# Performance work log

Hardware: AMD Instinct MI355X
Metric: run time of the kernel (lower is better)

## Reference

```python
import jax, jax.numpy as jnp
import numpy as np

K = 20  # neighbors, from init kwarg k

def _knn_idx(x, k):
    # x: [B, C, N]; returns indices of k nearest neighbors [B, N, k]
    xx = jnp.sum(x * x, axis=1)                      # [B, N]
    inner = jnp.einsum('bcn,bcm->bnm', x, x)         # [B, N, N]
    neg_dist = 2.0 * inner - xx[:, :, None] - xx[:, None, :]
    return jax.lax.top_k(neg_dist, k)[1]


def _graph_feature(x, k):
    # x: [B, C, N] -> [B, N, k, 2C] = concat(neighbor - center, center)
    idx = _knn_idx(jax.lax.stop_gradient(x), k)
    xt = jnp.swapaxes(x, 1, 2)                       # [B, N, C]
    nb = jax.vmap(lambda pts, i: pts[i])(xt, idx)    # [B, N, k, C]
    ctr = jnp.broadcast_to(xt[:, :, None, :], nb.shape)
    return jnp.concatenate([nb - ctr, ctr], axis=-1)


def _edge_conv(x, layers, k):
    # x: [B, C, N]; layers: list of (w [Co,Ci], scale [Co], bias [Co])
    g = _graph_feature(x, k)                         # [B, N, k, 2C]
    for w, s, b in layers:
        g = jax.nn.leaky_relu(jnp.einsum('bnkc,oc->bnko', g, w) * s + b, 0.2)
    return jnp.swapaxes(jnp.max(g, axis=2), 1, 2)    # [B, Co, N]


def setup_inputs() -> dict:
    key = jax.random.key(0)
    ks = jax.random.split(key, 20)
    B, N = 2, 8192
    emb = 1024
    def w(k_, shape):
        fan_in = shape[1]
        return jax.random.normal(k_, shape, jnp.float32) * (1.0 / np.sqrt(fan_in))
    def sc(k_, c):
        return jax.random.uniform(k_, (c,), jnp.float32, 0.5, 1.5)
    def bi(k_, c):
        return jax.random.normal(k_, (c,), jnp.float32) * 0.1
    inp = {
        'points': jax.random.normal(ks[0], (B, N, 3), jnp.float32),
        'w1a': w(ks[1], (64, 12)),  's1a': sc(ks[2], 64),  'b1a': bi(ks[3], 64),
        'w1b': w(ks[4], (64, 64)),  's1b': sc(ks[5], 64),  'b1b': bi(ks[6], 64),
        'w2a': w(ks[7], (64, 128)), 's2a': sc(ks[8], 64),  'b2a': bi(ks[9], 64),
        'w2b': w(ks[10], (64, 64)), 's2b': sc(ks[11], 64), 'b2b': bi(ks[12], 64),
        'w3a': w(ks[13], (64, 128)),'s3a': sc(ks[14], 64), 'b3a': bi(ks[15], 64),
        'wg':  w(ks[16], (emb, 192)),'sg': sc(ks[17], emb),'bg': bi(ks[18], emb),
    }
    return inp


def reference(points, w1a, s1a, b1a, w1b, s1b, b1b,
              w2a, s2a, b2a, w2b, s2b, b2b,
              w3a, s3a, b3a, wg, sg, bg):
    B, N, _ = points.shape
    xyz = jnp.swapaxes(points, 1, 2)                 # [B, 3, N]
    x = jnp.concatenate([xyz, xyz], axis=1)          # [B, 6, N] (features == xyz when C==3)
    x1 = _edge_conv(x,  [(w1a, s1a, b1a), (w1b, s1b, b1b)], K)
    x2 = _edge_conv(x1, [(w2a, s2a, b2a), (w2b, s2b, b2b)], K)
    x3 = _edge_conv(x2, [(w3a, s3a, b3a)], K)
    cat = jnp.concatenate([x1, x2, x3], axis=1)      # [B, 192, N]
    h = jax.nn.leaky_relu(
        jnp.einsum('bcn,oc->bon', cat, wg) * sg[None, :, None] + bg[None, :, None], 0.2)
    g = jnp.max(h, axis=-1, keepdims=True)           # [B, emb, 1]
    x_max = jnp.broadcast_to(g, (B, h.shape[1], N))  # [B, emb, N]
    return x_max
```

## Files before the change

### kernel.cpp

```cpp
#include <hip/hip_runtime.h>
#include <hip/hip_bf16.h>

#define NPTS 8192
#define KNN  20
#define KC   4

__device__ __forceinline__ unsigned fkey(float f) {
  unsigned u = __float_as_uint(f);
  return (u & 0x80000000u) ? ~u : (u | 0x80000000u);
}
__device__ __forceinline__ float funkey(unsigned k) {
  return (k & 0x80000000u) ? __uint_as_float(k & 0x7fffffffu) : __uint_as_float(~k);
}
__device__ __forceinline__ float lrelu(float x) { return x >= 0.f ? x : 0.2f * x; }

__global__ __launch_bounds__(256) void prep_kernel(
    const float* __restrict__ w1a, const float* __restrict__ w1b,
    const float* __restrict__ w2a, const float* __restrict__ w2b,
    const float* __restrict__ w3a, const float* __restrict__ wg,
    float* __restrict__ wp1A, float* __restrict__ wp1B,
    float* __restrict__ wp2A, float* __restrict__ wp2B,
    float* __restrict__ wp3A, float* __restrict__ wgT)
{
  const int t0 = blockIdx.x * blockDim.x + threadIdx.x;
  const int NT = gridDim.x * blockDim.x;
  for (int f = t0; f < 512; f += NT) {
    int i = f & 3, o = (f >> 2) & 63, c4 = f >> 8, c = c4 * 4 + i;
    float v = 0.f;
    if (c < 3)      v = w1a[o*12 + c]     + w1a[o*12 + c + 3];
    else if (c < 6) v = w1a[o*12 + c + 3] + w1a[o*12 + c + 6];
    wp1A[f] = v;
  }
  for (int f = t0; f < 4096; f += NT) {
    int i = f & 3, o = (f >> 2) & 63, c4 = f >> 8, c = c4 * 4 + i;
    wp1B[f] = w1b[o*64 + c];
    wp2B[f] = w2b[o*64 + c];
  }
  for (int f = t0; f < 8192; f += NT) {
    int i = f & 3, o = (f >> 2) & 63, c4 = f >> 8, c = c4 * 4 + i;
    wp2A[f] = w2a[o*128 + c];
    wp3A[f] = w3a[o*128 + c];
  }
  for (int f = t0; f < 192 * 1024; f += NT) {
    int c = f >> 10, o = f & 1023;
    wgT[f] = wg[o*192 + c];
  }
}

__global__ __launch_bounds__(256) void xx_points(const float* __restrict__ pts,
                                                 float* __restrict__ xx)
{
  int t = blockIdx.x * 256 + threadIdx.x;
  if (t < 2 * NPTS) {
    const float* p = pts + (size_t)t * 3;
    xx[t] = p[0]*p[0] + p[1]*p[1] + p[2]*p[2];
  }
}

__device__ __forceinline__ void bitonic64_desc_f(float& v, int lane) {
  #pragma unroll
  for (int k = 2; k <= 64; k <<= 1) {
    #pragma unroll
    for (int j = k >> 1; j >= 1; j >>= 1) {
      float o = __shfl_xor(v, j);
      bool take_max = (((lane & k) == 0) == ((lane & j) == 0));
      v = take_max ? fmaxf(v, o) : fminf(v, o);
    }
  }
}

__device__ __forceinline__ void bitonic64_desc_u64(unsigned long long& v, int lane) {
  #pragma unroll
  for (int k = 2; k <= 64; k <<= 1) {
    #pragma unroll
    for (int j = k >> 1; j >= 1; j >>= 1) {
      unsigned long long o = __shfl_xor(v, j);
      bool take_max = (((lane & k) == 0) == ((lane & j) == 0));
      unsigned long long hi = v > o ? v : o;
      unsigned long long lo = v > o ? o : v;
      v = take_max ? hi : lo;
    }
  }
}

__device__ void sel20_half(float* __restrict__ sdh, int half, int lane,
                           float* __restrict__ hv, int* __restrict__ hj,
                           float* __restrict__ cv, int* __restrict__ cj)
{
  float m = -INFINITY;
  const float4* rp = (const float4*)(sdh + lane * 64);
  #pragma unroll
  for (int t = 0; t < 16; ++t) {
    float4 x = rp[(t + lane) & 15];
    m = fmaxf(m, fmaxf(fmaxf(x.x, x.y), fmaxf(x.z, x.w)));
  }
  bitonic64_desc_f(m, lane);
  float That = __shfl(m, 19);

  int base = 0;
  for (int i = 0; i < 64; ++i) {
    float v = sdh[i * 64 + lane];
    bool p = (v >= That);
    unsigned long long mk = __ballot(p);
    if (p) {
      int pos = base + (int)__popcll(mk & ((1ull << lane) - 1ull));
      if (pos < 64) { cv[pos] = v; cj[pos] = i * 64 + lane; }
    }
    base += (int)__popcll(mk);
  }

  if (base <= 64) {
    unsigned long long key = 0ull;
    if (lane < base)
      key = (((unsigned long long)fkey(cv[lane])) << 32) | (unsigned)(~cj[lane]);
    bitonic64_desc_u64(key, lane);
    if (lane < KNN) {
      hv[lane] = funkey((unsigned)(key >> 32));
      hj[lane] = (half << 12) + (int)((~(unsigned)key) & 4095u);
    }
  } else {
    for (int kk = 0; kk < KNN; ++kk) {
      float bv = -INFINITY; int bj = 4096;
      for (int i = 0; i < 64; ++i) {
        float v = sdh[i * 64 + lane];
        if (v > bv) { bv = v; bj = i * 64 + lane; }
      }
      #pragma unroll
      for (int mm = 32; mm >= 1; mm >>= 1) {
        float ov = __shfl_xor(bv, mm); int oj = __shfl_xor(bj, mm);
        if (ov > bv || (ov == bv && oj < bj)) { bv = ov; bj = oj; }
      }
      if (lane == 0) { hv[kk] = bv; hj[kk] = (half << 12) + bj; }
      sdh[bj] = -INFINITY;
    }
  }
}

__device__ __forceinline__ void merge_halves(const float* __restrict__ hv,
                                             const int* __restrict__ hj,
                                             int lane, int* __restrict__ orow)
{
  unsigned long long key = 0ull;
  if (lane < 2 * KNN)
    key = (((unsigned long long)fkey(hv[lane])) << 32) | (unsigned)(~hj[lane]);
  bitonic64_desc_u64(key, lane);
  if (lane < KNN) orow[lane] = (int)((~(unsigned)key) & (NPTS - 1));
}

__device__ unsigned long long sel20_quarter(float* __restrict__ sdq, int jbase,
                                            int lane, float* __restrict__ cv,
                                            int* __restrict__ cj)
{
  float m = -INFINITY;
  #pragma unroll 8
  for (int i = 0; i < 32; ++i) m = fmaxf(m, sdq[i * 64 + lane]);
  bitonic64_desc_f(m, lane);
  float That = __shfl(m, 19);

  int base = 0;
  for (int i = 0; i < 32; ++i) {
    float v = sdq[i * 64 + lane];
    bool p = (v >= That);
    unsigned long long mk = __ballot(p);
    if (p) {
      int pos = base + (int)__popcll(mk & ((1ull << lane) - 1ull));
      if (pos < 64) { cv[pos] = v; cj[pos] = jbase + i * 64 + lane; }
    }
    base += (int)__popcll(mk);
  }

  unsigned long long key = 0ull;
  if (base <= 64) {
    if (lane < base)
      key = (((unsigned long long)fkey(cv[lane])) << 32) | (unsigned)(~cj[lane]);
    bitonic64_desc_u64(key, lane);
  } else {
    for (int kk = 0; kk < KNN; ++kk) {
      float bv = -INFINITY; int bj = 2048;
      for (int i = 0; i < 32; ++i) {
        float v = sdq[i * 64 + lane];
        if (v > bv) { bv = v; bj = i * 64 + lane; }
      }
      #pragma unroll
      for (int mm = 32; mm >= 1; mm >>= 1) {
        float ov = __shfl_xor(bv, mm); int oj = __shfl_xor(bj, mm);
        if (ov > bv || (ov == bv && oj < bj)) { bv = ov; bj = oj; }
      }
      if (lane == kk)
        key = (((unsigned long long)fkey(bv)) << 32) | (unsigned)(~(jbase + bj));
      sdq[bj] = -INFINITY;
    }
  }
  return key;
}

__global__ __launch_bounds__(512, 4) void knn3_kernel(
    const float* __restrict__ pts, const float* __restrict__ xx,
    int* __restrict__ idxout)
{
  __shared__ __align__(16) float sd[4][4096];
  __shared__ float s_ctr[4][4];
  __shared__ float s_hv[4][2 * KNN];
  __shared__ int   s_hj[4][2 * KNN];
  __shared__ float s_cv[4][64];
  __shared__ int   s_cj[4][64];
  const int tid = threadIdx.x;
  const int b   = blockIdx.x / (NPTS / 4);
  const int r0  = (blockIdx.x % (NPTS / 4)) * 4;
  const size_t rowbase = (size_t)b * NPTS;

  for (int i = tid; i < 12; i += 512)
    s_ctr[i / 3][i % 3] = pts[(rowbase + r0 + i / 3) * 3 + i % 3];
  __syncthreads();

  const float xr0 = xx[rowbase + r0 + 0], xr1 = xx[rowbase + r0 + 1];
  const float xr2 = xx[rowbase + r0 + 2], xr3 = xx[rowbase + r0 + 3];
  const float c00 = s_ctr[0][0], c01 = s_ctr[0][1], c02 = s_ctr[0][2];
  const float c10 = s_ctr[1][0], c11 = s_ctr[1][1], c12 = s_ctr[1][2];
  const float c20 = s_ctr[2][0], c21 = s_ctr[2][1], c22 = s_ctr[2][2];
  const float c30 = s_ctr[3][0], c31 = s_ctr[3][1], c32 = s_ctr[3][2];
  const int wid = tid >> 6, lane = tid & 63;

  #pragma unroll 1
  for (int h = 0; h < 2; ++h) {
    for (int jl = tid; jl < 4096; jl += 512) {
      const int jg = (h << 12) + jl;
      const float* fj = pts + (rowbase + jg) * 3;
      const float f0 = fj[0], f1 = fj[1], f2 = fj[2];
      const float xj = xx[rowbase + jg];
      sd[0][jl] = 2.f*(f0*c00 + f1*c01 + f2*c02) - xr0 - xj;
      sd[1][jl] = 2.f*(f0*c10 + f1*c11 + f2*c12) - xr1 - xj;
      sd[2][jl] = 2.f*(f0*c20 + f1*c21 + f2*c22) - xr2 - xj;
      sd[3][jl] = 2.f*(f0*c30 + f1*c31 + f2*c32) - xr3 - xj;
    }
    __syncthreads();
    if (wid < 4)
      sel20_half(sd[wid], h, lane, &s_hv[wid][h * KNN], &s_hj[wid][h * KNN],
                 s_cv[wid], s_cj[wid]);
    __syncthreads();
  }
  if (wid < 4)
    merge_halves(s_hv[wid], s_hj[wid], lane, idxout + (rowbase + r0 + wid) * KNN);
}

#define ACC4(A, C) \
  A.x += v0.x*C.x + v1.x*C.y + v2.x*C.z + v3.x*C.w; \
  A.y += v0.y*C.x + v1.y*C.y + v2.y*C.z + v3.y*C.w; \
  A.z += v0.z*C.x + v1.z*C.y + v2.z*C.z + v3.z*C.w; \
  A.w += v0.w*C.x + v1.w*C.y + v2.w*C.z + v3.w*C.w;

__global__ __launch_bounds__(512, 4) void knn64_kernel(
    const float* __restrict__ featT, const float* __restrict__ xx,
    int* __restrict__ idxout)
{
  __shared__ __align__(16) float sd[8][2048];
  __shared__ __align__(16) float s_ctr[8][64];
  __shared__ float s_cv[8][64];
  __shared__ int   s_cj[8][64];
  const int tid = threadIdx.x;
  const int bid = blockIdx.x;
  const int b   = (bid & 7) >> 2;
  const int r0  = (((bid >> 3) << 2) + (bid & 3)) * 8;
  const size_t tb = (size_t)b * 64 * NPTS;
  const size_t rowbase = (size_t)b * NPTS;

  s_ctr[tid >> 6][tid & 63] = featT[tb + (size_t)(tid & 63) * NPTS + r0 + (tid >> 6)];
  __syncthreads();

  const int wid = tid >> 6, lane = tid & 63;
  float xr[8];
  #pragma unroll
  for (int r = 0; r < 8; ++r) xr[r] = xx[rowbase + r0 + r];
  const float4* ct0 = (const float4*)s_ctr[0];
  const float4* ct1 = (const float4*)s_ctr[1];
  const float4* ct2 = (const float4*)s_ctr[2];
  const float4* ct3 = (const float4*)s_ctr[3];
  const float4* ct4 = (const float4*)s_ctr[4];
  const float4* ct5 = (const float4*)s_ctr[5];
  const float4* ct6 = (const float4*)s_ctr[6];
  const float4* ct7 = (const float4*)s_ctr[7];

  unsigned long long runkey = 0ull;

  #pragma unroll 1
  for (int h = 0; h < 4; ++h) {
    const int jl = (wid << 8) + (lane << 2);
    const int jg = (h << 11) + jl;
    float4 a0 = {0.f,0.f,0.f,0.f}, a1 = a0, a2 = a0, a3 = a0;
    float4 a4 = a0, a5 = a0, a6 = a0, a7 = a0;
    const float* fp0 = featT + tb + jg;
    #pragma unroll 2
    for (int c4 = 0; c4 < 16; ++c4) {
      const float* fp = fp0 + (size_t)(c4 * 4) * NPTS;
      float4 v0 = *(const float4*)(fp);
      float4 v1 = *(const float4*)(fp + NPTS);
      float4 v2 = *(const float4*)(fp + 2 * NPTS);
      float4 v3 = *(const float4*)(fp + 3 * NPTS);
      float4 c;
      c = ct0[c4]; ACC4(a0, c);
      c = ct1[c4]; ACC4(a1, c);
      c = ct2[c4]; ACC4(a2, c);
      c = ct3[c4]; ACC4(a3, c);
      c = ct4[c4]; ACC4(a4, c);
      c = ct5[c4]; ACC4(a5, c);
      c = ct6[c4]; ACC4(a6, c);
      c = ct7[c4]; ACC4(a7, c);
    }
    const float4 xv = *(const float4*)(xx + rowbase + jg);
    float4 s;
    #define STORE_ROW(A, R) \
      s.x = 2.f*A.x - xr[R] - xv.x; s.y = 2.f*A.y - xr[R] - xv.y; \
      s.z = 2.f*A.z - xr[R] - xv.z; s.w = 2.f*A.w - xr[R] - xv.w; \
      *(float4*)&sd[R][jl] = s;
    STORE_ROW(a0, 0); STORE_ROW(a1, 1); STORE_ROW(a2, 2); STORE_ROW(a3, 3);
    STORE_ROW(a4, 4); STORE_ROW(a5, 5); STORE_ROW(a6, 6); STORE_ROW(a7, 7);
    #undef STORE_ROW
    __syncthreads();

    unsigned long long pk = sel20_quarter(sd[wid], h << 11, lane,
                                          s_cv[wid], s_cj[wid]);
    unsigned long long nk = __shfl(pk, lane - 20);
    unsigned long long mkey = (lane < 20) ? runkey
                            : ((lane < 40) ? nk : 0ull);
    bitonic64_desc_u64(mkey, lane);
    runkey = mkey;
    __syncthreads();
  }
  if (lane < KNN)
    idxout[(rowbase + r0 + wid) * KNN + lane] =
        (int)((~(unsigned)runkey) & (NPTS - 1));
}

template<int D, bool HASB, bool WAUX>
__global__ __launch_bounds__(512, 2) void fused_conv(
    const float* __restrict__ feat, int fstride, int foff,
    const int* __restrict__ idx,
    const float4* __restrict__ wAp, const float* __restrict__ sa, const float* __restrict__ ba,
    const float4* __restrict__ wBp, const float* __restrict__ sb, const float* __restrict__ bb,
    float* __restrict__ outbuf, int ooff, float* __restrict__ xxout,
    float* __restrict__ featT)
{
  constexpr int CHA  = (D == 64) ? 32 : 2;
  constexpr int CHA4 = CHA * 4;
  __shared__ float4 s_wA[CHA * 64];
  __shared__ float4 s_wB[HASB ? 16 * 64 : 1];
  __shared__ __align__(16) float4 s_g[8 * KC * CHA];
  __shared__ __align__(16) float  s_h1[HASB ? 8 * KC * 64 : 4];
  __shared__ float s_ctr[8][(D > 4) ? D : 4];
  __shared__ float s_sa[64], s_ba[64], s_sb[64], s_bb[64];

  const int tid = threadIdx.x;
  const int p = tid >> 6, o = tid & 63;
  const int b  = blockIdx.x / (NPTS / 8);
  const int p0 = (blockIdx.x % (NPTS / 8)) * 8;
  const size_t rowbase = (size_t)b * NPTS;

  for (int i = tid; i < CHA * 64; i += 512) s_wA[i] = wAp[i];
  if (HASB) for (int i = tid; i < 16 * 64; i += 512) s_wB[i] = wBp[i];
  if (tid < 64) {
    s_sa[tid] = sa[tid]; s_ba[tid] = ba[tid];
    if (HASB) { s_sb[tid] = sb[tid]; s_bb[tid] = bb[tid]; }
  }
  for (int i = tid; i < 8 * D; i += 512)
    s_ctr[i / D][i % D] = feat[(rowbase + p0 + (i / D)) * fstride + foff + (i % D)];
  __syncthreads();

  float* s_gf = (float*)s_g;
  float hmax = -INFINITY;
  for (int kc = 0; kc < KNN / KC; ++kc) {
    for (int s = tid; s < 8 * KC * CHA4; s += 512) {
      int pp = s / (KC * CHA4);
      int rr = s - pp * (KC * CHA4);
      int kk = rr / CHA4;
      int c  = rr - kk * CHA4;
      int nb = idx[(rowbase + p0 + pp) * KNN + kc * KC + kk];
      float v;
      if (D == 64) {
        v = (c < 64) ? (feat[(rowbase + nb) * fstride + foff + c] - s_ctr[pp][c])
                     : s_ctr[pp][c - 64];
      } else {
        if (c < 3)      v = feat[(rowbase + nb) * 3 + c] - s_ctr[pp][c];
        else if (c < 6) v = s_ctr[pp][c - 3];
        else            v = 0.f;
      }
      s_gf[s] = v;
    }
    __syncthreads();

    float acc[KC];
    #pragma unroll
    for (int kk = 0; kk < KC; ++kk) acc[kk] = 0.f;
    for (int c4 = 0; c4 < CHA; ++c4) {
      float4 w = s_wA[c4 * 64 + o];
      #pragma unroll
      for (int kk = 0; kk < KC; ++kk) {
        float4 g = s_g[(p * KC + kk) * CHA + c4];
        acc[kk] += w.x*g.x + w.y*g.y + w.z*g.z + w.w*g.w;
      }
    }
    if (HASB) {
      #pragma unroll
      for (int kk = 0; kk < KC; ++kk)
        s_h1[(p * KC + kk) * 64 + o] = lrelu(acc[kk] * s_sa[o] + s_ba[o]);
      __syncthreads();
      float acc2[KC];
      #pragma unroll
      for (int kk = 0; kk < KC; ++kk) acc2[kk] = 0.f;
      const float4* s_h14 = (const float4*)s_h1;
      for (int c4 = 0; c4 < 16; ++c4) {
        float4 w = s_wB[c4 * 64 + o];
        #pragma unroll
        for (int kk = 0; kk < KC; ++kk) {
          float4 h = s_h14[(p * KC + kk) * 16 + c4];
          acc2[kk] += w.x*h.x + w.y*h.y + w.z*h.z + w.w*h.w;
        }
      }
      #pragma unroll
      for (int kk = 0; kk < KC; ++kk)
        hmax = fmaxf(hmax, lrelu(acc2[kk] * s_sb[o] + s_bb[o]));
      __syncthreads();
    } else {
      #pragma unroll
      for (int kk = 0; kk < KC; ++kk)
        hmax = fmaxf(hmax, lrelu(acc[kk] * s_sa[o] + s_ba[o]));
      __syncthreads();
    }
  }
  outbuf[(rowbase + p0 + p) * 192 + ooff + o] = hmax;
  if (WAUX) {
    featT[(size_t)b * 64 * NPTS + (size_t)o * NPTS + (p0 + p)] = hmax;
    float ss = hmax * hmax;
    #pragma unroll
    for (int m = 1; m < 64; m <<= 1) ss += __shfl_xor(ss, m);
    if (o == 0) xxout[rowbase + p0 + p] = ss;
  }
}

__global__ __launch_bounds__(256) void init_gmax(unsigned* __restrict__ g)
{
  int t = blockIdx.x * 256 + threadIdx.x;
  if (t < 2048) g[t] = fkey(-1e30f);
}

__global__ __launch_bounds__(256) void final_kernel(
    const float* __restrict__ cat, const float* __restrict__ wgT,
    const float* __restrict__ sg, const float* __restrict__ bg,
    unsigned* __restrict__ gmax)
{
  const int tid = threadIdx.x;
  const int chunk = blockIdx.x & 15;
  const int grp   = blockIdx.x >> 4;
  const int pt = grp * 256 + tid;
  const int b  = pt >> 13;
  const float4* crow = (const float4*)(cat + (size_t)pt * 192);
  float acc[64];
  #pragma unroll
  for (int o = 0; o < 64; ++o) acc[o] = 0.f;
  for (int c4 = 0; c4 < 48; ++c4) {
    float4 cv = crow[c4];
    const float* w0 = wgT + (size_t)(c4 * 4) * 1024 + chunk * 64;
    const float* w1 = w0 + 1024;
    const float* w2 = w1 + 1024;
    const float* w3 = w2 + 1024;
    #pragma unroll
    for (int o = 0; o < 64; ++o)
      acc[o] += cv.x*w0[o] + cv.y*w1[o] + cv.z*w2[o] + cv.w*w3[o];
  }
  const int lane = tid & 63;
  #pragma unroll
  for (int o = 0; o < 64; ++o) {
    int ch = chunk * 64 + o;
    float h = lrelu(acc[o] * sg[ch] + bg[ch]);
    #pragma unroll
    for (int m = 1; m < 64; m <<= 1) h = fmaxf(h, __shfl_xor(h, m));
    if (lane == 0) atomicMax(&gmax[b * 1024 + ch], fkey(h));
  }
}

__global__ __launch_bounds__(256) void bcast_kernel(const unsigned* __restrict__ gmax,
                                                    float* __restrict__ out)
{
  int t = blockIdx.x * 256 + threadIdx.x;
  int bo = t >> 11;
  float v = funkey(gmax[bo]);
  float4 w; w.x = v; w.y = v; w.z = v; w.w = v;
  ((float4*)out)[t] = w;
}

extern "C" void kernel_launch(void* const* d_in, const int* in_sizes, int n_in,
                              void* d_out, int out_size, void* d_ws, size_t ws_size,
                              hipStream_t stream)
{
  const float* points = (const float*)d_in[0];
  const float* w1a = (const float*)d_in[1];  const float* s1a = (const float*)d_in[2];  const float* b1a = (const float*)d_in[3];
  const float* w1b = (const float*)d_in[4];  const float* s1b = (const float*)d_in[5];  const float* b1b = (const float*)d_in[6];
  const float* w2a = (const float*)d_in[7];  const float* s2a = (const float*)d_in[8];  const float* b2a = (const float*)d_in[9];
  const float* w2b = (const float*)d_in[10]; const float* s2b = (const float*)d_in[11]; const float* b2b = (const float*)d_in[12];
  const float* w3a = (const float*)d_in[13]; const float* s3a = (const float*)d_in[14]; const float* b3a = (const float*)d_in[15];
  const float* wg  = (const float*)d_in[16]; const float* sg  = (const float*)d_in[17]; const float* bg  = (const float*)d_in[18];

  char* ws = (char*)d_ws;
  float*    cat   = (float*)(ws);
  float*    xxbuf = (float*)(ws + 12582912);
  int*      idxb  = (int*)  (ws + 12648448);
  float*    wp1A  = (float*)(ws + 13959168);
  float*    wp1B  = (float*)(ws + 13961216);
  float*    wp2A  = (float*)(ws + 13977600);
  float*    wp2B  = (float*)(ws + 14010368);
  float*    wp3A  = (float*)(ws + 14026752);
  float*    wgT   = (float*)(ws + 14059520);
  unsigned* gmax  = (unsigned*)(ws + 14845952);
  const size_t WS_NEED = 14854144;
  if (ws_size < WS_NEED || n_in != 19) return;

  float* featT = (float*)d_out;

  prep_kernel<<<256, 256, 0, stream>>>(w1a, w1b, w2a, w2b, w3a, wg,
                                       wp1A, wp1B, wp2A, wp2B, wp3A, wgT);
  xx_points<<<64, 256, 0, stream>>>(points, xxbuf);
  knn3_kernel<<<4096, 512, 0, stream>>>(points, xxbuf, idxb);
  fused_conv<3, true, true><<<2048, 512, 0, stream>>>(
      points, 3, 0, idxb, (const float4*)wp1A, s1a, b1a,
      (const float4*)wp1B, s1b, b1b, cat, 0, xxbuf, featT);
  knn64_kernel<<<2048, 512, 0, stream>>>(featT, xxbuf, idxb);
  fused_conv<64, true, true><<<2048, 512, 0, stream>>>(
      cat, 192, 0, idxb, (const float4*)wp2A, s2a, b2a,
      (const float4*)wp2B, s2b, b2b, cat, 64, xxbuf, featT);
  knn64_kernel<<<2048, 512, 0, stream>>>(featT, xxbuf, idxb);
  fused_conv<64, false, false><<<2048, 512, 0, stream>>>(
      cat, 192, 64, idxb, (const float4*)wp3A, s3a, b3a,
      nullptr, nullptr, nullptr, cat, 128, nullptr, nullptr);
  init_gmax<<<8, 256, 0, stream>>>(gmax);
  final_kernel<<<1024, 256, 0, stream>>>(cat, wgT, sg, bg, gmax);
  bcast_kernel<<<16384, 256, 0, stream>>>(gmax, (float*)d_out);
}
```

Before: 1.679 ms.

## Restructure knn3 to eight rows per block with quarter-tiled running top-k merge

The 3-D kNN kernel now handles eight query rows per block instead of four, so all eight waves do selection rather than only four. Candidate columns are processed in four 2048-wide quarters, and each quarter's top-20 is merged into a running register key with a bitonic sort. The distance fill now uses vectorized float4 loads and stores. Together these aim to raise wave utilization and halve the number of blocks that recompute the point loads, at the cost of more selection and merge passes per row.

```diff
diff --git a/kernel.cpp b/kernel.cpp
--- a/kernel.cpp
+++ b/kernel.cpp
@@ -81,70 +81,6 @@
       v = take_max ? hi : lo;
     }
   }
-}
-
-__device__ void sel20_half(float* __restrict__ sdh, int half, int lane,
-                           float* __restrict__ hv, int* __restrict__ hj,
-                           float* __restrict__ cv, int* __restrict__ cj)
-{
-  float m = -INFINITY;
-  const float4* rp = (const float4*)(sdh + lane * 64);
-  #pragma unroll
-  for (int t = 0; t < 16; ++t) {
-    float4 x = rp[(t + lane) & 15];
-    m = fmaxf(m, fmaxf(fmaxf(x.x, x.y), fmaxf(x.z, x.w)));
-  }
-  bitonic64_desc_f(m, lane);
-  float That = __shfl(m, 19);
-
-  int base = 0;
-  for (int i = 0; i < 64; ++i) {
-    float v = sdh[i * 64 + lane];
-    bool p = (v >= That);
-    unsigned long long mk = __ballot(p);
-    if (p) {
-      int pos = base + (int)__popcll(mk & ((1ull << lane) - 1ull));
-      if (pos < 64) { cv[pos] = v; cj[pos] = i * 64 + lane; }
-    }
-    base += (int)__popcll(mk);
-  }
-
-  if (base <= 64) {
-    unsigned long long key = 0ull;
-    if (lane < base)
-      key = (((unsigned long long)fkey(cv[lane])) << 32) | (unsigned)(~cj[lane]);
-    bitonic64_desc_u64(key, lane);
-    if (lane < KNN) {
-      hv[lane] = funkey((unsigned)(key >> 32));
-      hj[lane] = (half << 12) + (int)((~(unsigned)key) & 4095u);
-    }
-  } else {
-    for (int kk = 0; kk < KNN; ++kk) {
-      float bv = -INFINITY; int bj = 4096;
-      for (int i = 0; i < 64; ++i) {
-        float v = sdh[i * 64 + lane];
-        if (v > bv) { bv = v; bj = i * 64 + lane; }
-      }
-      #pragma unroll
-      for (int mm = 32; mm >= 1; mm >>= 1) {
-        float ov = __shfl_xor(bv, mm); int oj = __shfl_xor(bj, mm);
-        if (ov > bv || (ov == bv && oj < bj)) { bv = ov; bj = oj; }
-      }
-      if (lane == 0) { hv[kk] = bv; hj[kk] = (half << 12) + bj; }
-      sdh[bj] = -INFINITY;
-    }
-  }
-}
-
-__device__ __forceinline__ void merge_halves(const float* __restrict__ hv,
-                                             const int* __restrict__ hj,
-                                             int lane, int* __restrict__ orow)
-{
-  unsigned long long key = 0ull;
-  if (lane < 2 * KNN)
-    key = (((unsigned long long)fkey(hv[lane])) << 32) | (unsigned)(~hj[lane]);
-  bitonic64_desc_u64(key, lane);
-  if (lane < KNN) orow[lane] = (int)((~(unsigned)key) & (NPTS - 1));
 }
 
 __device__ unsigned long long sel20_quarter(float* __restrict__ sdq, int jbase,
@@ -198,49 +134,62 @@
     const float* __restrict__ pts, const float* __restrict__ xx,
     int* __restrict__ idxout)
 {
-  __shared__ __align__(16) float sd[4][4096];
-  __shared__ float s_ctr[4][4];
-  __shared__ float s_hv[4][2 * KNN];
-  __shared__ int   s_hj[4][2 * KNN];
-  __shared__ float s_cv[4][64];
-  __shared__ int   s_cj[4][64];
+  __shared__ __align__(16) float sd[8][2048];
+  __shared__ float s_ctr[8][4];
+  __shared__ float s_cv[8][64];
+  __shared__ int   s_cj[8][64];
   const int tid = threadIdx.x;
-  const int b   = blockIdx.x / (NPTS / 4);
-  const int r0  = (blockIdx.x % (NPTS / 4)) * 4;
+  const int bid = blockIdx.x;
+  const int b   = (bid & 7) >> 2;
+  const int r0  = (((bid >> 3) << 2) + (bid & 3)) * 8;
   const size_t rowbase = (size_t)b * NPTS;
 
-  for (int i = tid; i < 12; i += 512)
-    s_ctr[i / 3][i % 3] = pts[(rowbase + r0 + i / 3) * 3 + i % 3];
+  if (tid < 24)
+    s_ctr[tid / 3][tid % 3] = pts[(rowbase + r0 + tid / 3) * 3 + tid % 3];
   __syncthreads();
 
-  const float xr0 = xx[rowbase + r0 + 0], xr1 = xx[rowbase + r0 + 1];
-  const float xr2 = xx[rowbase + r0 + 2], xr3 = xx[rowbase + r0 + 3];
-  const float c00 = s_ctr[0][0], c01 = s_ctr[0][1], c02 = s_ctr[0][2];
-  const float c10 = s_ctr[1][0], c11 = s_ctr[1][1], c12 = s_ctr[1][2];
-  const float c20 = s_ctr[2][0], c21 = s_ctr[2][1], c22 = s_ctr[2][2];
-  const float c30 = s_ctr[3][0], c31 = s_ctr[3][1], c32 = s_ctr[3][2];
   const int wid = tid >> 6, lane = tid & 63;
+  float cx[8], cy[8], cz[8], xr[8];
+  #pragma unroll
+  for (int r = 0; r < 8; ++r) {
+    cx[r] = s_ctr[r][0]; cy[r] = s_ctr[r][1]; cz[r] = s_ctr[r][2];
+    xr[r] = xx[rowbase + r0 + r];
+  }
+
+  unsigned long long runkey = 0ull;
 
   #pragma unroll 1
-  for (int h = 0; h < 2; ++h) {
-    for (int jl = tid; jl < 4096; jl += 512) {
-      const int jg = (h << 12) + jl;
-      const float* fj = pts + (rowbase + jg) * 3;
-      const float f0 = fj[0], f1 = fj[1], f2 = fj[2];
-      const float xj = xx[rowbase + jg];
-      sd[0][jl] = 2.f*(f0*c00 + f1*c01 + f2*c02) - xr0 - xj;
-      sd[1][jl] = 2.f*(f0*c10 + f1*c11 + f2*c12) - xr1 - xj;
-      sd[2][jl] = 2.f*(f0*c20 + f1*c21 + f2*c22) - xr2 - xj;
-      sd[3][jl] = 2.f*(f0*c30 + f1*c31 + f2*c32) - xr3 - xj;
+  for (int h = 0; h < 4; ++h) {
+    const int jl = (wid << 8) + (lane << 2);
+    const int jg = (h << 11) + jl;
+    const float* pp = pts + (rowbase + jg) * 3;
+    float4 q0 = *(const float4*)(pp);
+    float4 q1 = *(const float4*)(pp + 4);
+    float4 q2 = *(const float4*)(pp + 8);
+    const float4 xv = *(const float4*)(xx + rowbase + jg);
+    #pragma unroll
+    for (int r = 0; r < 8; ++r) {
+      float4 s;
+      s.x = 2.f*(q0.x*cx[r] + q0.y*cy[r] + q0.z*cz[r]) - xr[r] - xv.x;
+      s.y = 2.f*(q0.w*cx[r] + q1.x*cy[r] + q1.y*cz[r]) - xr[r] - xv.y;
+      s.z = 2.f*(q1.z*cx[r] + q1.w*cy[r] + q2.x*cz[r]) - xr[r] - xv.z;
+      s.w = 2.f*(q2.y*cx[r] + q2.z*cy[r] + q2.w*cz[r]) - xr[r] - xv.w;
+      *(float4*)&sd[r][jl] = s;
     }
     __syncthreads();
-    if (wid < 4)
-      sel20_half(sd[wid], h, lane, &s_hv[wid][h * KNN], &s_hj[wid][h * KNN],
-                 s_cv[wid], s_cj[wid]);
+
+    unsigned long long pk = sel20_quarter(sd[wid], h << 11, lane,
+                                          s_cv[wid], s_cj[wid]);
+    unsigned long long nk = __shfl(pk, lane - 20);
+    unsigned long long mkey = (lane < 20) ? runkey
+                            : ((lane < 40) ? nk : 0ull);
+    bitonic64_desc_u64(mkey, lane);
+    runkey = mkey;
     __syncthreads();
   }
-  if (wid < 4)
-    merge_halves(s_hv[wid], s_hj[wid], lane, idxout + (rowbase + r0 + wid) * KNN);
+  if (lane < KNN)
+    idxout[(rowbase + r0 + wid) * KNN + lane] =
+        (int)((~(unsigned)runkey) & (NPTS - 1));
 }
 
 #define ACC4(A, C) \
@@ -518,7 +467,7 @@
   prep_kernel<<<256, 256, 0, stream>>>(w1a, w1b, w2a, w2b, w3a, wg,
                                        wp1A, wp1B, wp2A, wp2B, wp3A, wgT);
   xx_points<<<64, 256, 0, stream>>>(points, xxbuf);
-  knn3_kernel<<<4096, 512, 0, stream>>>(points, xxbuf, idxb);
+  knn3_kernel<<<2048, 512, 0, stream>>>(points, xxbuf, idxb);
   fused_conv<3, true, true><<<2048, 512, 0, stream>>>(
       points, 3, 0, idxb, (const float4*)wp1A, s1a, b1a,
       (const float4*)wp1B, s1b, b1b, cat, 0, xxbuf, featT);
```

Measured after the change: 1.826 ms. +8.8%, slower.
